# Kernel tuning notes

Hardware: AMD Instinct MI355X
Metric: run time of the kernel (lower is better)

## Reference

```python
import jax, jax.numpy as jnp
import numpy as np

N_LAYERS = 8
DILATIONS = [1, 2, 1, 2, 1, 2, 1, 2]
K_HOPS = 3
BN = 13248   # batch(64) * n_nodes(207), merged as in the torch module
L = 13       # 12 history steps + 1; shrinks by sum(dilations)=12 across layers
E = 211968   # BN * avg_degree(16)


def _conv1d(x, w, b, dil):
    # x: (BN, Cin, L), w: (Cout, Cin, 2) kernel-2 dilated conv, VALID (causal shrink)
    y = jax.lax.conv_general_dilated(x, w, (1,), 'VALID', rhs_dilation=(dil,),
                                     dimension_numbers=('NCH', 'OIH', 'NCH'))
    return y + b[None, :, None]


def setup_inputs() -> dict:
    key = jax.random.key(0)
    ks = jax.random.split(key, 20)
    s = 0.1  # keep activations in a sane range
    return {
        'x': jax.random.normal(ks[0], (BN, L, 2), jnp.float32),
        'edge_src': jax.random.randint(ks[1], (E,), 0, BN),
        'edge_dst': jax.random.randint(ks[2], (E,), 0, BN),
        'edge_w': jax.random.uniform(ks[3], (E,), jnp.float32),
        'init_w': s * jax.random.normal(ks[4], (2, 32), jnp.float32),
        'init_b': s * jax.random.normal(ks[5], (32,), jnp.float32),
        'filt_w': s * jax.random.normal(ks[6], (8, 32, 32, 2), jnp.float32),
        'filt_b': s * jax.random.normal(ks[7], (8, 32), jnp.float32),
        'gate_w': s * jax.random.normal(ks[8], (8, 32, 32, 2), jnp.float32),
        'gate_b': s * jax.random.normal(ks[9], (8, 32), jnp.float32),
        'gcn_w': s * jax.random.normal(ks[10], (8, 6, 32, 32), jnp.float32),
        'gcn_b': s * jax.random.normal(ks[11], (8, 32), jnp.float32),
        'skip_w': s * jax.random.normal(ks[12], (8, 256, 32), jnp.float32),
        'skip_b': s * jax.random.normal(ks[13], (8, 256), jnp.float32),
        'out0_w': s * jax.random.normal(ks[14], (256, 512), jnp.float32),
        'out0_b': s * jax.random.normal(ks[15], (512,), jnp.float32),
        'out1_w': s * jax.random.normal(ks[16], (512, 12), jnp.float32),
        'out1_b': s * jax.random.normal(ks[17], (12,), jnp.float32),
    }


def reference(x, edge_src, edge_dst, edge_w, init_w, init_b,
              filt_w, filt_b, gate_w, gate_b, gcn_w, gcn_b,
              skip_w, skip_b, out0_w, out0_b, out1_w, out1_b):
    # init linear: (BN, L, 2) -> (BN, L, 32) -> (BN, 32, L)
    h = (x @ init_w + init_b).transpose(0, 2, 1)
    # per-hop edge weights: elementwise powers of the transition weights
    # (faithful to repo's dense_to_sparse(transition ** k)); bck = transposed edges
    adjs = [(edge_src, edge_dst, edge_w ** k) for k in range(1, K_HOPS + 1)] + \
           [(edge_dst, edge_src, edge_w ** k) for k in range(1, K_HOPS + 1)]
    skip = None
    for l in range(N_LAYERS):
        d = DILATIONS[l]
        res = h
        # Gated TCN: tanh(filter) * sigmoid(gate), seq shrinks by d
        t = jnp.tanh(_conv1d(h, filt_w[l], filt_b[l], d)) * \
            jax.nn.sigmoid(_conv1d(h, gate_w[l], gate_b[l], d))
        # Diffusion conv: sum over 6 adjacency types of A_w (x W_a)
        xt = t.transpose(0, 2, 1)  # (BN, L', 32)
        g = jnp.zeros_like(xt)
        for a, (src, dst, w) in enumerate(adjs):
            msg = (xt @ gcn_w[l, a])[src] * w[:, None, None]  # (E, L', 32)
            g = g + jax.ops.segment_sum(msg, dst, num_segments=BN)
        h = g.transpose(0, 2, 1) + gcn_b[l][None, :, None]  # (BN, 32, L')
        # residual connection (align shrunk sequence)
        h = h + res[:, :, -h.shape[-1]:]
        # skip conv (1x1) on last timestep, accumulated
        sc = h[:, :, -1] @ skip_w[l].T + skip_b[l]  # (BN, 256)
        skip = sc if skip is None else skip + sc
    out = jax.nn.relu(skip)
    out = jax.nn.relu(out @ out0_w + out0_b)
    return out @ out1_w + out1_b  # (BN, 12)
```

## Files before the change

### kernel.cpp

```cpp
#include <hip/hip_runtime.h>
#include <hip/hip_fp16.h>

#define BN 13248
#define NE 211968
#define NBKT 8
#define SCAN_TOT (BN * NBKT)
#define SCAN_NBLK 52
#define ZSTRIDE 200
#define HSTRIDE 40

typedef __attribute__((ext_vector_type(8))) short bf16x8;
typedef __attribute__((ext_vector_type(8))) _Float16 f16x8;
typedef __attribute__((ext_vector_type(4))) float f32x4;

__device__ __forceinline__ f32x4 mfma16b(bf16x8 a, bf16x8 b, f32x4 c) {
  return __builtin_amdgcn_mfma_f32_16x16x32_bf16(a, b, c, 0, 0, 0);
}
__device__ __forceinline__ f32x4 mfma16h(f16x8 a, f16x8 b, f32x4 c) {
  return __builtin_amdgcn_mfma_f32_16x16x32_f16(a, b, c, 0, 0, 0);
}

__device__ __forceinline__ unsigned short to_bf16(float v) {
  unsigned bits = __float_as_uint(v);
  return (unsigned short)((bits + 0x7FFFu + ((bits >> 16) & 1u)) >> 16);
}
__device__ __forceinline__ unsigned short to_f16(float v) {
  union { __half h; unsigned short s; } u; u.h = __float2half(v); return u.s;
}
__device__ __forceinline__ unsigned h2u(__half2 h) {
  union { __half2 h; unsigned u; } v; v.h = h; return v.u;
}
__device__ __forceinline__ __half2 u2h(unsigned u) {
  union { unsigned u; __half2 h; } v; v.u = u; return v.h;
}

__device__ __forceinline__ float fast_tanh(float x) {
  float e2 = __expf(2.f * x);
  return 1.f - 2.f / (e2 + 1.f);
}
__device__ __forceinline__ float fast_sig(float x) {
  return 1.f / (1.f + __expf(-x));
}

template<int N>
__device__ __forceinline__ void vmwait() {
  if constexpr (N == 0)       asm volatile("s_waitcnt vmcnt(0)" ::: "memory");
  else if constexpr (N == 7)  asm volatile("s_waitcnt vmcnt(7)" ::: "memory");
  else if constexpr (N == 14) asm volatile("s_waitcnt vmcnt(14)" ::: "memory");
  else if constexpr (N == 21) asm volatile("s_waitcnt vmcnt(21)" ::: "memory");
  __builtin_amdgcn_sched_barrier(0);
}

template<int NJ>
__device__ __forceinline__ void stage_edge(const unsigned short* t_in, int node,
                                           char* stg, int slot, int lane) {
  const char* g = (const char*)t_in + (size_t)node * (NJ * 256);
  char* l = stg + slot * (NJ * 256);
#pragma unroll
  for (int j = 0; j < NJ; ++j)
    __builtin_amdgcn_global_load_lds(
        (const __attribute__((address_space(1))) void*)(g + j * 256 + lane * 4),
        (__attribute__((address_space(3))) void*)(l + j * 256), 4, 0, 0);
}

__device__ __forceinline__ void stage_ce(const int4* ce, int4* celds, int g, int lane) {
  __builtin_amdgcn_global_load_lds(
      (const __attribute__((address_space(1))) void*)(ce + g * 64 + lane),
      (__attribute__((address_space(3))) void*)(celds + g * 64), 16, 0, 0);
}

template<int NJ>
__device__ __forceinline__ void consume_edge(const char* stg, int slot,
                                             const int4* celds, int i, int lane, __half2* A) {
  int4 cw = celds[i];
  __half2 w1 = u2h((unsigned)cw.y), w2 = u2h((unsigned)cw.z), w3 = u2h((unsigned)cw.w);
  const char* sp = stg + slot * (NJ * 256);
#pragma unroll
  for (int j = 0; j < NJ; ++j) {
    __half2 v = *(const __half2*)(sp + (j * 64 + lane) * 4);
    A[0 * NJ + j] = __hfma2(w1, v, A[0 * NJ + j]);
    A[1 * NJ + j] = __hfma2(w2, v, A[1 * NJ + j]);
    A[2 * NJ + j] = __hfma2(w3, v, A[2 * NJ + j]);
  }
}

__global__ void k_count(const int* __restrict__ src, const int* __restrict__ dst,
                        int* __restrict__ cur_f, int* __restrict__ cur_b) {
  int e = blockIdx.x * 256 + threadIdx.x;
  if (e < NE) {
    int s = src[e], t = dst[e];
    atomicAdd(&cur_f[t * NBKT + (s >> 11)], 1);
    atomicAdd(&cur_b[s * NBKT + (t >> 11)], 1);
  }
}

__global__ __launch_bounds__(1024) void k_scan1(int* __restrict__ cnt_f, int* __restrict__ cnt_b,
                                                int* __restrict__ bsum) {
  __shared__ int sdata[1024];
  int b = blockIdx.x;
  int dir = (b >= SCAN_NBLK) ? 1 : 0;
  int lb = dir ? b - SCAN_NBLK : b;
  int* cnt = dir ? cnt_b : cnt_f;
  int tid = threadIdx.x;
  int i0 = lb * 2048 + tid * 2;
  int v0 = (i0 < SCAN_TOT) ? cnt[i0] : 0;
  int v1 = (i0 + 1 < SCAN_TOT) ? cnt[i0 + 1] : 0;
  int tot = v0 + v1;
  sdata[tid] = tot;
  __syncthreads();
  for (int off = 1; off < 1024; off <<= 1) {
    int add = (tid >= off) ? sdata[tid - off] : 0;
    __syncthreads();
    sdata[tid] += add;
    __syncthreads();
  }
  int excl = sdata[tid] - tot;
  if (i0 < SCAN_TOT) cnt[i0] = excl;
  if (i0 + 1 < SCAN_TOT) cnt[i0 + 1] = excl + v0;
  if (tid == 1023) bsum[b] = sdata[1023];
}

__global__ void k_scan2(int* __restrict__ bsum) {
  __shared__ int sdata[128];
  int tid = threadIdx.x;
  int seg = (tid >= 64) ? 64 : 0;
  int src = (tid < 64) ? tid : tid - 64 + SCAN_NBLK;
  int valid = ((tid & 63) < SCAN_NBLK);
  int v = valid ? bsum[src] : 0;
  sdata[tid] = v;
  __syncthreads();
  for (int off = 1; off < 64; off <<= 1) {
    int add = (tid - off >= seg) ? sdata[tid - off] : 0;
    __syncthreads();
    sdata[tid] += add;
    __syncthreads();
  }
  if (valid) bsum[src] = sdata[tid] - v;
}

__global__ __launch_bounds__(1024) void k_scan3(int* __restrict__ cnt_f, int* __restrict__ cnt_b,
                                                const int* __restrict__ bsum,
                                                int* __restrict__ row_f, int* __restrict__ row_b) {
  int b = blockIdx.x;
  int dir = (b >= SCAN_NBLK) ? 1 : 0;
  int lb = dir ? b - SCAN_NBLK : b;
  int* cnt = dir ? cnt_b : cnt_f;
  int* row = dir ? row_b : row_f;
  int off = bsum[b];
  int tid = threadIdx.x;
#pragma unroll
  for (int k = 0; k < 2; ++k) {
    int idx = lb * 2048 + tid * 2 + k;
    if (idx < SCAN_TOT) {
      int v = cnt[idx] + off;
      cnt[idx] = v;
      if ((idx & (NBKT - 1)) == 0) row[idx / NBKT] = v;
    }
  }
  if (b == 0 && tid == 0) { row_f[BN] = NE; row_b[BN] = NE; }
}

__global__ void k_fill(const int* __restrict__ src, const int* __restrict__ dst,
                       const float* __restrict__ w,
                       int* __restrict__ cur_f, int4* __restrict__ ce_f,
                       int* __restrict__ cur_b, int4* __restrict__ ce_b) {
  int e = blockIdx.x * 256 + threadIdx.x;
  if (e < NE) {
    int s = src[e], t = dst[e];
    float wv = w[e];
    float w2 = wv * wv, w3 = w2 * wv;
    int u1 = (int)h2u(__float2half2_rn(wv));
    int u2 = (int)h2u(__float2half2_rn(w2));
    int u3 = (int)h2u(__float2half2_rn(w3));
    int p = atomicAdd(&cur_f[t * NBKT + (s >> 11)], 1); ce_f[p] = make_int4(s, u1, u2, u3);
    int q = atomicAdd(&cur_b[s * NBKT + (t >> 11)], 1); ce_b[q] = make_int4(t, u1, u2, u3);
  }
}

__global__ void k_init(const float* __restrict__ x, const float* __restrict__ iw,
                       const float* __restrict__ ib, float* __restrict__ h) {
  int idx = blockIdx.x * 256 + threadIdx.x;
  if (idx >= BN * 13 * 32) return;
  int c = idx & 31;
  int r = idx >> 5;
  int n = r % BN;
  int tau = r / BN;
  float x0 = x[(n * 13 + tau) * 2 + 0];
  float x1 = x[(n * 13 + tau) * 2 + 1];
  h[idx] = fmaf(x0, iw[c], fmaf(x1, iw[32 + c], ib[c]));
}

__global__ void k_pack(const float* __restrict__ skip_w, const float* __restrict__ skip_b,
                       const float* __restrict__ w0, const float* __restrict__ w1,
                       const float* __restrict__ gcn_w,
                       const float* __restrict__ filt_w, const float* __restrict__ gate_w,
                       unsigned short* __restrict__ SWb, unsigned short* __restrict__ W0T,
                       unsigned short* __restrict__ W1T, float* __restrict__ bsum,
                       unsigned short* __restrict__ Gg16, unsigned short* __restrict__ WTC) {
  int id = blockIdx.x * 256 + threadIdx.x;
  if (id < 65536) {
    int j = id >> 8, k = id & 255;
    SWb[id] = to_bf16(skip_w[((k >> 5) * 256 + j) * 32 + (k & 31)]);
  }
  if (id < 131072) {
    int jo = id >> 8, k = id & 255;
    W0T[id] = to_bf16(w0[k * 512 + jo]);
  }
  if (id < 8192) {
    int n = id >> 9, k = id & 511;
    W1T[id] = (n < 12) ? to_bf16(w1[k * 12 + n]) : (unsigned short)0;
  }
  if (id < 256) {
    float s = 0.f;
    for (int l = 0; l < 8; ++l) s += skip_b[l * 256 + id];
    bsum[id] = s;
  }
  if (id < 49152) {
    int l = id / 6144, rem = id % 6144;
    int co = rem / 192, k = rem % 192;
    int a = k >> 5, ci = k & 31;
    Gg16[id] = to_f16(gcn_w[((l * 6 + a) * 32 + ci) * 32 + co]);
  }
  if (id < 32768) {
    int l = id >> 12, rem = id & 4095;
    int g = rem >> 11, co = (rem >> 6) & 31, k = rem & 63;
    const float* srcw = (g ? gate_w : filt_w) + l * 2048;
    float v = (k < 32) ? srcw[(co * 32 + k) * 2 + 0] : srcw[(co * 32 + (k - 32)) * 2 + 1];
    WTC[id] = to_f16(v);
  }
}

template<int LIN, int D, int TPAD>
__global__ __launch_bounds__(256) void k_tcn(const float* __restrict__ h_in, unsigned short* __restrict__ t_out,
    const float* __restrict__ fw, const float* __restrict__ fb,
    const float* __restrict__ gw, const float* __restrict__ gb) {
  constexpr int LOUT = LIN - D;
  __shared__ __align__(16) float wq[32 * 32 * 4];
  __shared__ float hl[8][LIN * 32];
  int tid = threadIdx.x;
  for (int f = tid; f < 4096; f += 256) {
    int e = f & 3, co = (f >> 2) & 31, ci = f >> 7;
    const float* srcw = (e < 2) ? fw : gw;
    wq[f] = srcw[(co * 32 + ci) * 2 + (e & 1)];
  }
  int n0 = blockIdx.x * 8;
  for (int i = tid; i < 8 * LIN * 32; i += 256) {
    int c = i & 31, r = i >> 5;
    int nl = r / LIN, tau = r % LIN;
    hl[nl][tau * 32 + c] = h_in[(tau * BN + n0 + nl) * 32 + c];
  }
  __syncthreads();
  int nl = tid >> 5, co = tid & 31;
  int n = n0 + nl;
  float accf[LOUT], accg[LOUT];
  float fbv = fb[co], gbv = gb[co];
#pragma unroll
  for (int j = 0; j < LOUT; ++j) { accf[j] = fbv; accg[j] = gbv; }
#pragma unroll
  for (int ci = 0; ci < 32; ++ci) {
    float4 wv = *(const float4*)&wq[(ci * 32 + co) * 4];
    float xr[LIN];
#pragma unroll
    for (int t = 0; t < LIN; ++t) xr[t] = hl[nl][t * 32 + ci];
#pragma unroll
    for (int j = 0; j < LOUT; ++j) {
      accf[j] = fmaf(xr[j], wv.x, accf[j]);
      accf[j] = fmaf(xr[j + D], wv.y, accf[j]);
      accg[j] = fmaf(xr[j], wv.z, accg[j]);
      accg[j] = fmaf(xr[j + D], wv.w, accg[j]);
    }
  }
#pragma unroll
  for (int j = 0; j < TPAD; ++j) {
    unsigned short v = 0;
    if (j < LOUT) v = to_f16(fast_tanh(accf[j < LOUT ? j : 0]) * fast_sig(accg[j < LOUT ? j : 0]));
    t_out[(n * TPAD + j) * 32 + co] = v;
  }
}

template<int LOUT, int D, int TPAD, int D2, int TPAD2, bool LAST>
__global__ __launch_bounds__(64, 6) void k_fused(
    const unsigned short* __restrict__ t_in,
    const float* __restrict__ h_in, float* __restrict__ h_out,
    float* __restrict__ lastcol, unsigned short* __restrict__ t_next,
    const int* __restrict__ row_f, const int4* __restrict__ ce_f,
    const int* __restrict__ row_b, const int4* __restrict__ ce_b,
    const unsigned short* __restrict__ Wg,
    const float* __restrict__ bias,
    const unsigned short* __restrict__ Wtc,
    const float* __restrict__ fbn, const float* __restrict__ gbn) {
  constexpr int NJ = TPAD / 4;
  constexpr int LOUT2 = LAST ? 1 : (LOUT - D2);
  constexpr int Q = 8;
  constexpr int CAP = 128;
  constexpr int BLKB = NJ * 256;
  constexpr int STAGEB = Q * BLKB;
  constexpr int GATB = STAGEB + CAP * 16;
  constexpr int ZB = 16 * ZSTRIDE * 2;
  constexpr int SBYTES = GATB > ZB ? GATB : ZB;
  __shared__ __align__(256) char smem[SBYTES];
  char* stg = smem;
  int4* celds = (int4*)(smem + STAGEB);
  unsigned short* Zl = (unsigned short*)smem;
  unsigned short* hb16 = (unsigned short*)smem;
  int lane = threadIdx.x;
  int n = blockIdx.x;
  __half2 acc[6 * NJ];
  __half2 zero = __float2half2_rn(0.f);
#pragma unroll
  for (int i = 0; i < 6 * NJ; ++i) acc[i] = zero;

#pragma unroll
  for (int dh = 0; dh < 2; ++dh) {
    const int* rowp = dh ? row_b : row_f;
    const int4* cebase = dh ? ce_b : ce_f;
    __half2* A = acc + dh * 3 * NJ;
    int e0 = rowp[n], e1 = rowp[n + 1];
    for (int c0 = e0; c0 < e1; c0 += CAP) {
      int cnt = min(e1 - c0, CAP);
      const int4* ce = cebase + c0;
      int ng = (cnt + 63) >> 6;
      for (int g = 0; g < ng; ++g) stage_ce(ce, celds, g, lane);
      vmwait<0>();
      if (cnt > Q) {
        int cols[Q];
#pragma unroll
        for (int k = 0; k < Q; ++k) cols[k] = celds[k].x;
#pragma unroll
        for (int k = 0; k < Q; ++k) stage_edge<NJ>(t_in, cols[k], stg, k, lane);
        int body = cnt - Q;
        for (int i = 0; i < body; ++i) {
          int nxt = celds[i + Q].x;
          vmwait<(Q - 1) * NJ>();
          consume_edge<NJ>(stg, i & (Q - 1), celds, i, lane, A);
          stage_edge<NJ>(t_in, nxt, stg, (i + Q) & (Q - 1), lane);
        }
        vmwait<0>();
        for (int i = body; i < cnt; ++i)
          consume_edge<NJ>(stg, i & (Q - 1), celds, i, lane, A);
      } else {
        for (int k = 0; k < cnt; ++k) stage_edge<NJ>(t_in, celds[k].x, stg, k, lane);
        vmwait<0>();
        for (int i = 0; i < cnt; ++i) consume_edge<NJ>(stg, i, celds, i, lane, A);
      }
    }
  }

#pragma unroll
  for (int j = 0; j < NJ; ++j) {
    int u = j * 64 + lane;
    int row = u >> 4, cp = u & 15;
#pragma unroll
    for (int a3 = 0; a3 < 6; ++a3)
      *(unsigned*)(&Zl[row * ZSTRIDE + a3 * 32 + cp * 2]) = h2u(acc[a3 * NJ + j]);
  }
  __syncthreads();

  int m16 = lane & 15, qq = lane >> 4;
  f32x4 dacc[2];
#pragma unroll
  for (int nt = 0; nt < 2; ++nt) {
    dacc[nt] = (f32x4){0.f, 0.f, 0.f, 0.f};
#pragma unroll
    for (int ks = 0; ks < 6; ++ks) {
      f16x8 av = *(const f16x8*)(&Zl[m16 * ZSTRIDE + ks * 32 + qq * 8]);
      f16x8 bv = *(const f16x8*)((const _Float16*)Wg + (nt * 16 + m16) * 192 + ks * 32 + qq * 8);
      dacc[nt] = mfma16h(av, bv, dacc[nt]);
    }
  }
  __syncthreads();
#pragma unroll
  for (int nt = 0; nt < 2; ++nt) {
    int co = nt * 16 + m16;
    float bco = bias[co];
#pragma unroll
    for (int r = 0; r < 4; ++r) {
      int tau = qq * 4 + r;
      if (tau < LOUT) {
        float rres = h_in[((tau + D) * BN + n) * 32 + co];
        float o = dacc[nt][r] + bco + rres;
        h_out[(tau * BN + n) * 32 + co] = o;
        if (!LAST) hb16[tau * HSTRIDE + co] = to_f16(o);
        if (tau == LOUT - 1) lastcol[n * 32 + co] = o;
      }
    }
  }
  if (!LAST) {
    __syncthreads();
#pragma unroll
    for (int i = 0; i < 2; ++i) {
      int co = i * 16 + m16;
      f32x4 df = (f32x4){0.f, 0.f, 0.f, 0.f};
      f32x4 dg = (f32x4){0.f, 0.f, 0.f, 0.f};
#pragma unroll
      for (int s = 0; s < 2; ++s) {
        f16x8 av = *(const f16x8*)(&hb16[(m16 + s * D2) * HSTRIDE + qq * 8]);
        f16x8 bvf = *(const f16x8*)((const _Float16*)Wtc + (0 * 32 + co) * 64 + s * 32 + qq * 8);
        f16x8 bvg = *(const f16x8*)((const _Float16*)Wtc + (1 * 32 + co) * 64 + s * 32 + qq * 8);
        df = mfma16h(av, bvf, df);
        dg = mfma16h(av, bvg, dg);
      }
      float fbv = fbn[co], gbv = gbn[co];
#pragma unroll
      for (int r = 0; r < 4; ++r) {
        int j = qq * 4 + r;
        if (j < TPAD2) {
          unsigned short v = 0;
          if (j < LOUT2)
            v = to_f16(fast_tanh(df[r] + fbv) * fast_sig(dg[r] + gbv));
          t_next[(n * TPAD2 + j) * 32 + co] = v;
        }
      }
    }
  }
}

__device__ __forceinline__ bf16x8 ldsA(const unsigned short* buf, int stride, int row, int ks, int q) {
  int unit = ks * 4 + q;
  int addr = row * stride + ((unit ^ (row & 7)) << 3);
  return *(const bf16x8*)(buf + addr);
}

__global__ __launch_bounds__(256) void k_final(const float* __restrict__ lastcol,
    const unsigned short* __restrict__ SWb, const unsigned short* __restrict__ W0T,
    const unsigned short* __restrict__ W1T, const float* __restrict__ bsum,
    const float* __restrict__ b0, const float* __restrict__ b1,
    float* __restrict__ out) {
  __shared__ __align__(16) unsigned short Z[32 * 256];
  __shared__ __align__(16) unsigned short H[32 * 512];
  int tid = threadIdx.x;
  int wave = tid >> 6, lane = tid & 63;
  int m16 = lane & 15, q = lane >> 4;
  int n0 = blockIdx.x * 32;
#pragma unroll
  for (int it = 0; it < 32; ++it) {
    int id = it * 256 + tid;
    int m = id >> 8, k = id & 255;
    float v = lastcol[((k >> 5) * BN + n0 + m) * 32 + (k & 31)];
    Z[m * 256 + (((k >> 3) ^ (m & 7)) << 3) + (k & 7)] = to_bf16(v);
  }
  __syncthreads();
  f32x4 acc1[2][4];
#pragma unroll
  for (int mt = 0; mt < 2; ++mt)
#pragma unroll
    for (int i = 0; i < 4; ++i) acc1[mt][i] = (f32x4){0.f, 0.f, 0.f, 0.f};
#pragma unroll
  for (int ks = 0; ks < 8; ++ks) {
    bf16x8 a0 = ldsA(Z, 256, m16, ks, q);
    bf16x8 a1 = ldsA(Z, 256, 16 + m16, ks, q);
#pragma unroll
    for (int i = 0; i < 4; ++i) {
      int j = (wave * 4 + i) * 16 + m16;
      bf16x8 b = *(const bf16x8*)(SWb + j * 256 + ks * 32 + q * 8);
      acc1[0][i] = mfma16b(a0, b, acc1[0][i]);
      acc1[1][i] = mfma16b(a1, b, acc1[1][i]);
    }
  }
  __syncthreads();
#pragma unroll
  for (int i = 0; i < 4; ++i) {
    int j = (wave * 4 + i) * 16 + m16;
    float bs = bsum[j];
#pragma unroll
    for (int mt = 0; mt < 2; ++mt)
#pragma unroll
      for (int r = 0; r < 4; ++r) {
        int row = mt * 16 + q * 4 + r;
        float v = fmaxf(acc1[mt][i][r] + bs, 0.f);
        Z[row * 256 + (((j >> 3) ^ (row & 7)) << 3) + (j & 7)] = to_bf16(v);
      }
  }
  __syncthreads();
  f32x4 acc2[2][8];
#pragma unroll
  for (int mt = 0; mt < 2; ++mt)
#pragma unroll
    for (int i = 0; i < 8; ++i) acc2[mt][i] = (f32x4){0.f, 0.f, 0.f, 0.f};
#pragma unroll
  for (int ks = 0; ks < 8; ++ks) {
    bf16x8 a0 = ldsA(Z, 256, m16, ks, q);
    bf16x8 a1 = ldsA(Z, 256, 16 + m16, ks, q);
#pragma unroll
    for (int i = 0; i < 8; ++i) {
      int jo = (wave * 8 + i) * 16 + m16;
      bf16x8 b = *(const bf16x8*)(W0T + jo * 256 + ks * 32 + q * 8);
      acc2[0][i] = mfma16b(a0, b, acc2[0][i]);
      acc2[1][i] = mfma16b(a1, b, acc2[1][i]);
    }
  }
#pragma unroll
  for (int i = 0; i < 8; ++i) {
    int jo = (wave * 8 + i) * 16 + m16;
    float b0v = b0[jo];
#pragma unroll
    for (int mt = 0; mt < 2; ++mt)
#pragma unroll
      for (int r = 0; r < 4; ++r) {
        int row = mt * 16 + q * 4 + r;
        float v = fmaxf(acc2[mt][i][r] + b0v, 0.f);
        H[row * 512 + (((jo >> 3) ^ (row & 7)) << 3) + (jo & 7)] = to_bf16(v);
      }
  }
  __syncthreads();
  if (wave < 2) {
    f32x4 acc3 = (f32x4){0.f, 0.f, 0.f, 0.f};
#pragma unroll
    for (int ks = 0; ks < 16; ++ks) {
      bf16x8 a = ldsA(H, 512, wave * 16 + m16, ks, q);
      bf16x8 b = *(const bf16x8*)(W1T + m16 * 512 + ks * 32 + q * 8);
      acc3 = mfma16b(a, b, acc3);
    }
    if (m16 < 12) {
      float bv = b1[m16];
#pragma unroll
      for (int r = 0; r < 4; ++r)
        out[(n0 + wave * 16 + q * 4 + r) * 12 + m16] = acc3[r] + bv;
    }
  }
}

extern "C" void kernel_launch(void* const* d_in, const int* in_sizes, int n_in,
                              void* d_out, int out_size, void* d_ws, size_t ws_size,
                              hipStream_t stream) {
  const float* x      = (const float*)d_in[0];
  const int*   esrc   = (const int*)d_in[1];
  const int*   edst   = (const int*)d_in[2];
  const float* ew     = (const float*)d_in[3];
  const float* init_w = (const float*)d_in[4];
  const float* init_b = (const float*)d_in[5];
  const float* filt_w = (const float*)d_in[6];
  const float* filt_b = (const float*)d_in[7];
  const float* gate_w = (const float*)d_in[8];
  const float* gate_b = (const float*)d_in[9];
  const float* gcn_w  = (const float*)d_in[10];
  const float* gcn_b  = (const float*)d_in[11];
  const float* skip_w = (const float*)d_in[12];
  const float* skip_b = (const float*)d_in[13];
  const float* w0     = (const float*)d_in[14];
  const float* b0     = (const float*)d_in[15];
  const float* w1     = (const float*)d_in[16];
  const float* b1     = (const float*)d_in[17];
  float* out = (float*)d_out;

  float* base = (float*)d_ws;
  float* hA      = base;
  float* hB      = hA + 13 * BN * 32;
  unsigned short* tA = (unsigned short*)(hB + 13 * BN * 32);
  unsigned short* tB = tA + 12 * BN * 32;
  float* lastcol = (float*)(tB + 12 * BN * 32);
  int* row_f = (int*)(lastcol + 8 * BN * 32);
  int* row_b = row_f + (BN + 2);
  int* bscan = row_b + (BN + 2);
  int* cur_f = bscan + 128;
  int* cur_b = cur_f + BN * NBKT;
  int4* ce_f = (int4*)(cur_b + BN * NBKT);
  int4* ce_b = ce_f + NE;
  unsigned short* SWb  = (unsigned short*)(ce_b + NE);
  unsigned short* W0T  = SWb + 65536;
  unsigned short* W1T  = W0T + 131072;
  unsigned short* Gg16 = W1T + 8192;
  unsigned short* WTC  = Gg16 + 49152;
  float* bsumv = (float*)(WTC + 32768);

  hipMemsetAsync(cur_f, 0, 2 * BN * NBKT * sizeof(int), stream);
  const int egrid = (NE + 255) / 256;
  k_count<<<egrid, 256, 0, stream>>>(esrc, edst, cur_f, cur_b);
  k_scan1<<<2 * SCAN_NBLK, 1024, 0, stream>>>(cur_f, cur_b, bscan);
  k_scan2<<<1, 128, 0, stream>>>(bscan);
  k_scan3<<<2 * SCAN_NBLK, 1024, 0, stream>>>(cur_f, cur_b, bscan, row_f, row_b);
  k_fill<<<egrid, 256, 0, stream>>>(esrc, edst, ew, cur_f, ce_f, cur_b, ce_b);
  k_init<<<(BN * 13 * 32 + 255) / 256, 256, 0, stream>>>(x, init_w, init_b, hA);
  k_pack<<<512, 256, 0, stream>>>(skip_w, skip_b, w0, w1, gcn_w, filt_w, gate_w,
                                  SWb, W0T, W1T, bsumv, Gg16, WTC);

  k_tcn<13, 1, 12><<<BN / 8, 256, 0, stream>>>(hA, tA, filt_w, filt_b, gate_w, gate_b);

#define FUSED(l, LOUTv, Dv, TPv, D2v, TP2v, LASTv, tin, tout, hin, hout) \
  k_fused<LOUTv, Dv, TPv, D2v, TP2v, LASTv><<<BN, 64, 0, stream>>>( \
      tin, hin, hout, lastcol + l * BN * 32, tout, row_f, ce_f, row_b, ce_b, \
      Gg16 + l * 6144, gcn_b + l * 32, WTC + (l + 1) * 4096, \
      filt_b + (l + 1) * 32, gate_b + (l + 1) * 32);

  FUSED(0, 12, 1, 12, 2, 12, false, tA, tB, hA, hB)
  FUSED(1, 10, 2, 12, 1, 12, false, tB, tA, hB, hA)
  FUSED(2,  9, 1, 12, 2,  8, false, tA, tB, hA, hB)
  FUSED(3,  7, 2,  8, 1,  8, false, tB, tA, hB, hA)
  FUSED(4,  6, 1,  8, 2,  4, false, tA, tB, hA, hB)
  FUSED(5,  4, 2,  4, 1,  4, false, tB, tA, hB, hA)
  FUSED(6,  3, 1,  4, 2,  4, false, tA, tB, hA, hB)
#undef FUSED
  k_fused<1, 2, 4, 2, 4, true><<<BN, 64, 0, stream>>>(
      tB, hB, hA, lastcol + 7 * BN * 32, tA, row_f, ce_f, row_b, ce_b,
      Gg16 + 7 * 6144, gcn_b + 7 * 32, WTC, filt_b, gate_b);

  k_final<<<BN / 32, 256, 0, stream>>>(lastcol, SWb, W0T, W1T, bsumv, b0, b1, out);
}
```

Measured before the change: 686.0 us.

## Process four nodes per wave with a continuous cross-node gather pipeline

Each 64-thread block now handles four consecutive nodes. The edge-gather prefetch queue runs continuously across the four nodes and both edge directions, so the pipeline no longer drains and refills at every node boundary. The queue depth rises from 8 to 12, block-wide barriers become wave-local LDS waits, and the launch-bounds occupancy hint drops to 2. LDS use per block grows, a fallback path handles nodes with oversized edge lists, and the ce buffers are padded so staging can read past the end safely.

```diff
diff --git a/kernel.cpp b/kernel.cpp
--- a/kernel.cpp
+++ b/kernel.cpp
@@ -45,9 +45,13 @@
 template<int N>
 __device__ __forceinline__ void vmwait() {
   if constexpr (N == 0)       asm volatile("s_waitcnt vmcnt(0)" ::: "memory");
-  else if constexpr (N == 7)  asm volatile("s_waitcnt vmcnt(7)" ::: "memory");
-  else if constexpr (N == 14) asm volatile("s_waitcnt vmcnt(14)" ::: "memory");
-  else if constexpr (N == 21) asm volatile("s_waitcnt vmcnt(21)" ::: "memory");
+  else if constexpr (N == 11) asm volatile("s_waitcnt vmcnt(11)" ::: "memory");
+  else if constexpr (N == 22) asm volatile("s_waitcnt vmcnt(22)" ::: "memory");
+  else if constexpr (N == 33) asm volatile("s_waitcnt vmcnt(33)" ::: "memory");
+  __builtin_amdgcn_sched_barrier(0);
+}
+__device__ __forceinline__ void wave_lds_fence() {
+  asm volatile("s_waitcnt lgkmcnt(0)" ::: "memory");
   __builtin_amdgcn_sched_barrier(0);
 }
 
@@ -279,7 +283,86 @@
 }
 
 template<int LOUT, int D, int TPAD, int D2, int TPAD2, bool LAST>
-__global__ __launch_bounds__(64, 6) void k_fused(
+__device__ __forceinline__ void do_node(__half2* acc, int n, int lane,
+    unsigned short* Zl,
+    const float* __restrict__ h_in, float* __restrict__ h_out,
+    float* __restrict__ lastcol, unsigned short* __restrict__ t_next,
+    const unsigned short* __restrict__ Wg, const float* __restrict__ bias,
+    const unsigned short* __restrict__ Wtc,
+    const float* __restrict__ fbn, const float* __restrict__ gbn) {
+  constexpr int NJ = TPAD / 4;
+  constexpr int LOUT2 = LAST ? 1 : (LOUT - D2);
+  unsigned short* hb16 = Zl;
+#pragma unroll
+  for (int j = 0; j < NJ; ++j) {
+    int u = j * 64 + lane;
+    int row = u >> 4, cp = u & 15;
+#pragma unroll
+    for (int a3 = 0; a3 < 6; ++a3)
+      *(unsigned*)(&Zl[row * ZSTRIDE + a3 * 32 + cp * 2]) = h2u(acc[a3 * NJ + j]);
+  }
+  wave_lds_fence();
+  int m16 = lane & 15, qq = lane >> 4;
+  f32x4 dacc[2];
+#pragma unroll
+  for (int nt = 0; nt < 2; ++nt) {
+    dacc[nt] = (f32x4){0.f, 0.f, 0.f, 0.f};
+#pragma unroll
+    for (int ks = 0; ks < 6; ++ks) {
+      f16x8 av = *(const f16x8*)(&Zl[m16 * ZSTRIDE + ks * 32 + qq * 8]);
+      f16x8 bv = *(const f16x8*)((const _Float16*)Wg + (nt * 16 + m16) * 192 + ks * 32 + qq * 8);
+      dacc[nt] = mfma16h(av, bv, dacc[nt]);
+    }
+  }
+  wave_lds_fence();
+#pragma unroll
+  for (int nt = 0; nt < 2; ++nt) {
+    int co = nt * 16 + m16;
+    float bco = bias[co];
+#pragma unroll
+    for (int r = 0; r < 4; ++r) {
+      int tau = qq * 4 + r;
+      if (tau < LOUT) {
+        float rres = h_in[((tau + D) * BN + n) * 32 + co];
+        float o = dacc[nt][r] + bco + rres;
+        h_out[(tau * BN + n) * 32 + co] = o;
+        if (!LAST) hb16[tau * HSTRIDE + co] = to_f16(o);
+        if (tau == LOUT - 1) lastcol[n * 32 + co] = o;
+      }
+    }
+  }
+  if (!LAST) {
+    wave_lds_fence();
+#pragma unroll
+    for (int i = 0; i < 2; ++i) {
+      int co = i * 16 + m16;
+      f32x4 df = (f32x4){0.f, 0.f, 0.f, 0.f};
+      f32x4 dg = (f32x4){0.f, 0.f, 0.f, 0.f};
+#pragma unroll
+      for (int s = 0; s < 2; ++s) {
+        f16x8 av = *(const f16x8*)(&hb16[(m16 + s * D2) * HSTRIDE + qq * 8]);
+        f16x8 bvf = *(const f16x8*)((const _Float16*)Wtc + (0 * 32 + co) * 64 + s * 32 + qq * 8);
+        f16x8 bvg = *(const f16x8*)((const _Float16*)Wtc + (1 * 32 + co) * 64 + s * 32 + qq * 8);
+        df = mfma16h(av, bvf, df);
+        dg = mfma16h(av, bvg, dg);
+      }
+      float fbv = fbn[co], gbv = gbn[co];
+#pragma unroll
+      for (int r = 0; r < 4; ++r) {
+        int j = qq * 4 + r;
+        if (j < TPAD2) {
+          unsigned short v = 0;
+          if (j < LOUT2)
+            v = to_f16(fast_tanh(df[r] + fbv) * fast_sig(dg[r] + gbv));
+          t_next[(n * TPAD2 + j) * 32 + co] = v;
+        }
+      }
+    }
+  }
+}
+
+template<int LOUT, int D, int TPAD, int D2, int TPAD2, bool LAST>
+__global__ __launch_bounds__(64, 2) void k_fused(
     const unsigned short* __restrict__ t_in,
     const float* __restrict__ h_in, float* __restrict__ h_out,
     float* __restrict__ lastcol, unsigned short* __restrict__ t_next,
@@ -290,127 +373,112 @@
     const unsigned short* __restrict__ Wtc,
     const float* __restrict__ fbn, const float* __restrict__ gbn) {
   constexpr int NJ = TPAD / 4;
-  constexpr int LOUT2 = LAST ? 1 : (LOUT - D2);
-  constexpr int Q = 8;
-  constexpr int CAP = 128;
-  constexpr int BLKB = NJ * 256;
-  constexpr int STAGEB = Q * BLKB;
-  constexpr int GATB = STAGEB + CAP * 16;
+  constexpr int Q = 12;
+  constexpr int CAPD = 128;
+  constexpr int SQB = Q * NJ * 256;
+  constexpr int CEB = CAPD * 16;
+  constexpr int ZOFF = SQB + 2 * CEB + 256;
   constexpr int ZB = 16 * ZSTRIDE * 2;
-  constexpr int SBYTES = GATB > ZB ? GATB : ZB;
-  __shared__ __align__(256) char smem[SBYTES];
+  __shared__ __align__(256) char smem[ZOFF + ZB];
   char* stg = smem;
-  int4* celds = (int4*)(smem + STAGEB);
-  unsigned short* Zl = (unsigned short*)smem;
-  unsigned short* hb16 = (unsigned short*)smem;
+  int4* cefL = (int4*)(smem + SQB);
+  int4* cebL = (int4*)(smem + SQB + CEB);
+  int* lrun = (int*)(smem + SQB + 2 * CEB);
+  unsigned short* Zl = (unsigned short*)(smem + ZOFF);
   int lane = threadIdx.x;
-  int n = blockIdx.x;
-  __half2 acc[6 * NJ];
+  int n0 = blockIdx.x * 4;
+  int rf0 = row_f[n0], rf4 = row_f[n0 + 4];
+  int rb0 = row_b[n0], rb4 = row_b[n0 + 4];
+  int cf = rf4 - rf0, cb = rb4 - rb0;
   __half2 zero = __float2half2_rn(0.f);
-#pragma unroll
-  for (int i = 0; i < 6 * NJ; ++i) acc[i] = zero;
-
-#pragma unroll
-  for (int dh = 0; dh < 2; ++dh) {
-    const int* rowp = dh ? row_b : row_f;
-    const int4* cebase = dh ? ce_b : ce_f;
-    __half2* A = acc + dh * 3 * NJ;
-    int e0 = rowp[n], e1 = rowp[n + 1];
-    for (int c0 = e0; c0 < e1; c0 += CAP) {
-      int cnt = min(e1 - c0, CAP);
-      const int4* ce = cebase + c0;
-      int ng = (cnt + 63) >> 6;
-      for (int g = 0; g < ng; ++g) stage_ce(ce, celds, g, lane);
-      vmwait<0>();
-      if (cnt > Q) {
-        int cols[Q];
-#pragma unroll
-        for (int k = 0; k < Q; ++k) cols[k] = celds[k].x;
-#pragma unroll
-        for (int k = 0; k < Q; ++k) stage_edge<NJ>(t_in, cols[k], stg, k, lane);
-        int body = cnt - Q;
-        for (int i = 0; i < body; ++i) {
-          int nxt = celds[i + Q].x;
-          vmwait<(Q - 1) * NJ>();
-          consume_edge<NJ>(stg, i & (Q - 1), celds, i, lane, A);
-          stage_edge<NJ>(t_in, nxt, stg, (i + Q) & (Q - 1), lane);
-        }
-        vmwait<0>();
-        for (int i = body; i < cnt; ++i)
-          consume_edge<NJ>(stg, i & (Q - 1), celds, i, lane, A);
-      } else {
-        for (int k = 0; k < cnt; ++k) stage_edge<NJ>(t_in, celds[k].x, stg, k, lane);
-        vmwait<0>();
-        for (int i = 0; i < cnt; ++i) consume_edge<NJ>(stg, i, celds, i, lane, A);
-      }
-    }
-  }
-
-#pragma unroll
-  for (int j = 0; j < NJ; ++j) {
-    int u = j * 64 + lane;
-    int row = u >> 4, cp = u & 15;
-#pragma unroll
-    for (int a3 = 0; a3 < 6; ++a3)
-      *(unsigned*)(&Zl[row * ZSTRIDE + a3 * 32 + cp * 2]) = h2u(acc[a3 * NJ + j]);
-  }
-  __syncthreads();
-
-  int m16 = lane & 15, qq = lane >> 4;
-  f32x4 dacc[2];
-#pragma unroll
-  for (int nt = 0; nt < 2; ++nt) {
-    dacc[nt] = (f32x4){0.f, 0.f, 0.f, 0.f};
-#pragma unroll
-    for (int ks = 0; ks < 6; ++ks) {
-      f16x8 av = *(const f16x8*)(&Zl[m16 * ZSTRIDE + ks * 32 + qq * 8]);
-      f16x8 bv = *(const f16x8*)((const _Float16*)Wg + (nt * 16 + m16) * 192 + ks * 32 + qq * 8);
-      dacc[nt] = mfma16h(av, bv, dacc[nt]);
-    }
-  }
-  __syncthreads();
-#pragma unroll
-  for (int nt = 0; nt < 2; ++nt) {
-    int co = nt * 16 + m16;
-    float bco = bias[co];
-#pragma unroll
-    for (int r = 0; r < 4; ++r) {
-      int tau = qq * 4 + r;
-      if (tau < LOUT) {
-        float rres = h_in[((tau + D) * BN + n) * 32 + co];
-        float o = dacc[nt][r] + bco + rres;
-        h_out[(tau * BN + n) * 32 + co] = o;
-        if (!LAST) hb16[tau * HSTRIDE + co] = to_f16(o);
-        if (tau == LOUT - 1) lastcol[n * 32 + co] = o;
-      }
-    }
-  }
-  if (!LAST) {
-    __syncthreads();
-#pragma unroll
-    for (int i = 0; i < 2; ++i) {
-      int co = i * 16 + m16;
-      f32x4 df = (f32x4){0.f, 0.f, 0.f, 0.f};
-      f32x4 dg = (f32x4){0.f, 0.f, 0.f, 0.f};
-#pragma unroll
-      for (int s = 0; s < 2; ++s) {
-        f16x8 av = *(const f16x8*)(&hb16[(m16 + s * D2) * HSTRIDE + qq * 8]);
-        f16x8 bvf = *(const f16x8*)((const _Float16*)Wtc + (0 * 32 + co) * 64 + s * 32 + qq * 8);
-        f16x8 bvg = *(const f16x8*)((const _Float16*)Wtc + (1 * 32 + co) * 64 + s * 32 + qq * 8);
-        df = mfma16h(av, bvf, df);
-        dg = mfma16h(av, bvg, dg);
-      }
-      float fbv = fbn[co], gbv = gbn[co];
-#pragma unroll
-      for (int r = 0; r < 4; ++r) {
-        int j = qq * 4 + r;
-        if (j < TPAD2) {
-          unsigned short v = 0;
-          if (j < LOUT2)
-            v = to_f16(fast_tanh(df[r] + fbv) * fast_sig(dg[r] + gbv));
-          t_next[(n * TPAD2 + j) * 32 + co] = v;
+
+  if (cf <= CAPD && cb <= CAPD) {
+    for (int g = 0; g * 64 < cf; ++g) stage_ce(ce_f + rf0, cefL, g, lane);
+    for (int g = 0; g * 64 < cb; ++g) stage_ce(ce_b + rb0, cebL, g, lane);
+    if (lane < 8) {
+      int node = lane >> 1, dir = lane & 1;
+      const int* rp = dir ? row_b : row_f;
+      int base = dir ? rb0 : rf0;
+      lrun[lane * 2 + 0] = rp[n0 + node] - base;
+      lrun[lane * 2 + 1] = rp[n0 + node + 1] - base;
+    }
+    wave_lds_fence();
+    vmwait<0>();
+    int sr = 0, si = lrun[0], shi = lrun[1];
+    while (sr < 8 && si >= shi) { ++sr; if (sr < 8) { si = lrun[sr * 2]; shi = lrun[sr * 2 + 1]; } }
+    int sslot = 0, primed = 0;
+    while (primed < Q && sr < 8) {
+      int col = ((sr & 1) ? cebL : cefL)[si].x;
+      stage_edge<NJ>(t_in, col, stg, sslot, lane);
+      if (++sslot == Q) sslot = 0;
+      ++primed; ++si;
+      while (sr < 8 && si >= shi) { ++sr; if (sr < 8) { si = lrun[sr * 2]; shi = lrun[sr * 2 + 1]; } }
+    }
+    int cslot = 0;
+    bool drained = false;
+    for (int nl = 0; nl < 4; ++nl) {
+      __half2 acc[6 * NJ];
+#pragma unroll
+      for (int i = 0; i < 6 * NJ; ++i) acc[i] = zero;
+      for (int dh = 0; dh < 2; ++dh) {
+        int r = nl * 2 + dh;
+        int lo = lrun[r * 2], hi = lrun[r * 2 + 1];
+        const int4* tab = dh ? cebL : cefL;
+        __half2* A = acc + dh * 3 * NJ;
+        for (int i = lo; i < hi; ++i) {
+          if (sr < 8) { vmwait<(Q - 1) * NJ>(); }
+          else if (!drained) { vmwait<0>(); drained = true; }
+          consume_edge<NJ>(stg, cslot, tab, i, lane, A);
+          if (++cslot == Q) cslot = 0;
+          if (sr < 8) {
+            int col = ((sr & 1) ? cebL : cefL)[si].x;
+            stage_edge<NJ>(t_in, col, stg, sslot, lane);
+            if (++sslot == Q) sslot = 0;
+            ++si;
+            while (sr < 8 && si >= shi) { ++sr; if (sr < 8) { si = lrun[sr * 2]; shi = lrun[sr * 2 + 1]; } }
+          }
         }
       }
+      do_node<LOUT, D, TPAD, D2, TPAD2, LAST>(acc, n0 + nl, lane, Zl,
+          h_in, h_out, lastcol, t_next, Wg, bias, Wtc, fbn, gbn);
+    }
+  } else {
+    for (int nl = 0; nl < 4; ++nl) {
+      __half2 acc[6 * NJ];
+#pragma unroll
+      for (int i = 0; i < 6 * NJ; ++i) acc[i] = zero;
+      for (int dh = 0; dh < 2; ++dh) {
+        const int* rowp = dh ? row_b : row_f;
+        const int4* cebase = dh ? ce_b : ce_f;
+        __half2* A = acc + dh * 3 * NJ;
+        int e0 = rowp[n0 + nl], e1 = rowp[n0 + nl + 1];
+        for (int c0 = e0; c0 < e1; c0 += CAPD) {
+          int cnt = min(e1 - c0, CAPD);
+          for (int g = 0; g * 64 < cnt; ++g) stage_ce(cebase + c0, cefL, g, lane);
+          vmwait<0>();
+          int P = cnt < Q ? cnt : Q;
+          int ss = 0, cs = 0;
+          for (int k = 0; k < P; ++k) {
+            stage_edge<NJ>(t_in, cefL[k].x, stg, ss, lane);
+            if (++ss == Q) ss = 0;
+          }
+          int body = cnt - P;
+          for (int i = 0; i < body; ++i) {
+            vmwait<(Q - 1) * NJ>();
+            consume_edge<NJ>(stg, cs, cefL, i, lane, A);
+            stage_edge<NJ>(t_in, cefL[i + P].x, stg, ss, lane);
+            if (++cs == Q) cs = 0;
+            if (++ss == Q) ss = 0;
+          }
+          vmwait<0>();
+          for (int i = body; i < cnt; ++i) {
+            consume_edge<NJ>(stg, cs, cefL, i, lane, A);
+            if (++cs == Q) cs = 0;
+          }
+        }
+      }
+      do_node<LOUT, D, TPAD, D2, TPAD2, LAST>(acc, n0 + nl, lane, Zl,
+          h_in, h_out, lastcol, t_next, Wg, bias, Wtc, fbn, gbn);
     }
   }
 }
@@ -555,8 +623,8 @@
   int* cur_f = bscan + 128;
   int* cur_b = cur_f + BN * NBKT;
   int4* ce_f = (int4*)(cur_b + BN * NBKT);
-  int4* ce_b = ce_f + NE;
-  unsigned short* SWb  = (unsigned short*)(ce_b + NE);
+  int4* ce_b = ce_f + NE + 128;
+  unsigned short* SWb  = (unsigned short*)(ce_b + NE + 128);
   unsigned short* W0T  = SWb + 65536;
   unsigned short* W1T  = W0T + 131072;
   unsigned short* Gg16 = W1T + 8192;
@@ -577,7 +645,7 @@
   k_tcn<13, 1, 12><<<BN / 8, 256, 0, stream>>>(hA, tA, filt_w, filt_b, gate_w, gate_b);
 
 #define FUSED(l, LOUTv, Dv, TPv, D2v, TP2v, LASTv, tin, tout, hin, hout) \
-  k_fused<LOUTv, Dv, TPv, D2v, TP2v, LASTv><<<BN, 64, 0, stream>>>( \
+  k_fused<LOUTv, Dv, TPv, D2v, TP2v, LASTv><<<BN / 4, 64, 0, stream>>>( \
       tin, hin, hout, lastcol + l * BN * 32, tout, row_f, ce_f, row_b, ce_b, \
       Gg16 + l * 6144, gcn_b + l * 32, WTC + (l + 1) * 4096, \
       filt_b + (l + 1) * 32, gate_b + (l + 1) * 32);
@@ -590,7 +658,7 @@
   FUSED(5,  4, 2,  4, 1,  4, false, tB, tA, hB, hA)
   FUSED(6,  3, 1,  4, 2,  4, false, tA, tB, hA, hB)
 #undef FUSED
-  k_fused<1, 2, 4, 2, 4, true><<<BN, 64, 0, stream>>>(
+  k_fused<1, 2, 4, 2, 4, true><<<BN / 4, 64, 0, stream>>>(
       tB, hB, hA, lastcol + 7 * BN * 32, tA, row_f, ce_f, row_b, ce_b,
       Gg16 + 7 * 6144, gcn_b + 7 * 32, WTC, filt_b, gate_b);
 
```

After: 1.127 ms. +64.3%, slower.
